# Optimization experiments

Measured on AMD Instinct MI355X. Metric: run time of the kernel, lower is better.

Reference implementation:

```python
import jax, jax.numpy as jnp
import numpy as np

IN_FEATURES = 8192
OUT_FEATURES = 14336
M_TOKENS = 64


def _dequant_rowwise_int4(w_packed, w_scales):
    # w_packed: [out, in//2], each byte holds two signed int4 values
    # (low nibble = even k index, high nibble = odd k index, two's complement)
    low = w_packed & 0xF
    high = (w_packed >> 4) & 0xF
    q = jnp.stack([low, high], axis=-1).reshape(w_packed.shape[0], -1)  # [out, in]
    q = jnp.where(q >= 8, q - 16, q).astype(jnp.float32)
    return q * w_scales[:, None]  # [out, in]


def setup_inputs() -> dict:
    key = jax.random.key(0)
    k1, k2, k3, k4 = jax.random.split(key, 4)
    x = jax.random.normal(k1, (M_TOKENS, IN_FEATURES), dtype=jnp.float32)
    w_packed = jax.random.randint(k2, (OUT_FEATURES, IN_FEATURES // 2), 0, 256, dtype=jnp.int32)
    # per-row scales, small positive values as produced by max-abs/7 quantization
    w_scales = jax.random.uniform(k3, (OUT_FEATURES,), dtype=jnp.float32) * 0.02 + 1e-4
    bias = jax.random.normal(k4, (OUT_FEATURES,), dtype=jnp.float32)
    return {"x": x, "w_packed": w_packed, "w_scales": w_scales, "bias": bias}


def reference(x, w_packed, w_scales, bias):
    original_shape = x.shape[:-1]
    x_2d = x.reshape(-1, IN_FEATURES)
    w = _dequant_rowwise_int4(w_packed, w_scales)  # [out, in]
    y = x_2d @ w.T + bias[None, :]  # [M, out]
    return y.reshape(*original_shape, OUT_FEATURES)
```

## Files before the change

### kernel.cpp

```cpp
#include <hip/hip_runtime.h>

#define IN_F   8192
#define OUT_F  14336
#define M_TOK  64
#define KPI    4096
#define BN     128
#define NBLK   (OUT_F / BN)
#define KSPLIT 8
#define KCHUNK (IN_F / KSPLIT)
#define BK     64
#define NSTEP  (KCHUNK / BK)
#define PSTRIDE (M_TOK * OUT_F)

typedef __attribute__((ext_vector_type(8)))  short bf16x8;
typedef __attribute__((ext_vector_type(16))) float f32x16;

__device__ __forceinline__ unsigned short f2bf_rne(float f) {
    unsigned u = __builtin_bit_cast(unsigned, f);
    u += 0x7FFFu + ((u >> 16) & 1u);
    return (unsigned short)(u >> 16);
}

__global__ __launch_bounds__(256) void qlin_prep(const float* __restrict__ x,
                                                 unsigned short* __restrict__ xb) {
    int gid = blockIdx.x * 256 + threadIdx.x;
    float4 v = reinterpret_cast<const float4*>(x)[gid];
    ushort4 o;
    o.x = f2bf_rne(v.x);
    o.y = f2bf_rne(v.y);
    o.z = f2bf_rne(v.z);
    o.w = f2bf_rne(v.w);
    reinterpret_cast<ushort4*>(xb)[gid] = o;
}

__device__ __forceinline__ int unpack2_bf16(int v) {
    int q0 = ((int)((unsigned)v << 28)) >> 28;
    int q1 = ((int)((unsigned)v << 24)) >> 28;
    unsigned u0 = __builtin_bit_cast(unsigned, (float)q0);
    unsigned u1 = __builtin_bit_cast(unsigned, (float)q1);
    return (int)((u0 >> 16) | (u1 & 0xFFFF0000u));
}

__device__ __forceinline__ bf16x8 unpack_b(int4 wv) {
    int4 pk;
    pk.x = unpack2_bf16(wv.x);
    pk.y = unpack2_bf16(wv.y);
    pk.z = unpack2_bf16(wv.z);
    pk.w = unpack2_bf16(wv.w);
    return __builtin_bit_cast(bf16x8, pk);
}

__device__ __forceinline__ void gload_lds16(const void* g, void* l) {
    __builtin_amdgcn_global_load_lds(
        (const __attribute__((address_space(1))) unsigned int*)g,
        (__attribute__((address_space(3))) unsigned int*)l,
        16, 0, 0);
}

__global__ __launch_bounds__(256) void qlin_gemm(const unsigned short* __restrict__ xb,
                                                 const int* __restrict__ wp,
                                                 const float* __restrict__ scales,
                                                 float* __restrict__ part) {
    __shared__ int            wlds[2][BN * (BK / 2)];
    __shared__ unsigned short xlds[2][M_TOK * BK];

    const int tid  = threadIdx.x;
    const int wave = tid >> 6;
    const int lane = tid & 63;
    const int tp   = lane & 31;
    const int qp   = lane >> 5;

    const int nblk = blockIdx.x % NBLK;
    const int kblk = blockIdx.x / NBLK;
    const int n0   = nblk * BN;
    const int kb   = kblk * KCHUNK;

    f32x16 acc0 = {0.f,0.f,0.f,0.f,0.f,0.f,0.f,0.f,0.f,0.f,0.f,0.f,0.f,0.f,0.f,0.f};
    f32x16 acc1 = acc0;

#define STAGE(b, t) do {                                                           \
    _Pragma("unroll")                                                              \
    for (int j = 0; j < 4; ++j) {                                                  \
        int li = (wave * 4 + j) * 64 + lane;                     \
        int r  = li >> 3;                                   \
        int cg = (li & 7) ^ (r & 7);                  \
        const int* gp = wp + (size_t)(n0 + r) * KPI + (kb >> 1) + (t) * (BK / 2) + cg * 4; \
        gload_lds16(gp, (char*)&wlds[b][0] + (size_t)li * 16);                     \
    }                                                                              \
    _Pragma("unroll")                                                              \
    for (int j = 0; j < 2; ++j) {                                                  \
        int li = (wave * 2 + j) * 64 + lane;                      \
        int r  = li >> 3;                                         \
        int cg = (li & 7) ^ (r & 7);                                               \
        const unsigned short* gp = xb + (size_t)r * IN_F + kb + (t) * BK + cg * 8; \
        gload_lds16(gp, (char*)&xlds[b][0] + (size_t)li * 16);                     \
    }                                                                              \
} while (0)

#define COMPUTE(b) do {                                                            \
    _Pragma("unroll")                                                              \
    for (int kf = 0; kf < 4; ++kf) {                                               \
        const int c = kf * 2 + qp;                      \
        const int R = wave * 32 + tp;                                              \
        int4 wv = *reinterpret_cast<const int4*>(                                  \
            (const char*)&wlds[b][0] + (size_t)(R * 8 + (c ^ (R & 7))) * 16);      \
        bf16x8 bb = unpack_b(wv);                                                  \
        bf16x8 a0 = *reinterpret_cast<const bf16x8*>(                              \
            (const char*)&xlds[b][0] + (size_t)(tp * 8 + (c ^ (tp & 7))) * 16);    \
        bf16x8 a1 = *reinterpret_cast<const bf16x8*>(                              \
            (const char*)&xlds[b][0] + (size_t)((32 + tp) * 8 + (c ^ (tp & 7))) * 16); \
        acc0 = __builtin_amdgcn_mfma_f32_32x32x16_bf16(a0, bb, acc0, 0, 0, 0);     \
        acc1 = __builtin_amdgcn_mfma_f32_32x32x16_bf16(a1, bb, acc1, 0, 0, 0);     \
    }                                                                              \
} while (0)

    STAGE(0, 0);
    STAGE(1, 1);

    for (int t = 0; t < NSTEP - 1; ++t) {
        const int cur = t & 1;
        asm volatile("s_waitcnt vmcnt(6)" ::: "memory");
        __builtin_amdgcn_sched_barrier(0);
        __builtin_amdgcn_s_barrier();
        __builtin_amdgcn_sched_barrier(0);
        COMPUTE(cur);
        __builtin_amdgcn_sched_barrier(0);
        __builtin_amdgcn_s_barrier();
        __builtin_amdgcn_sched_barrier(0);
        if (t + 2 < NSTEP) STAGE(cur, t + 2);
    }
    asm volatile("s_waitcnt vmcnt(0)" ::: "memory");
    __builtin_amdgcn_sched_barrier(0);
    __builtin_amdgcn_s_barrier();
    __builtin_amdgcn_sched_barrier(0);
    COMPUTE((NSTEP - 1) & 1);

    const int   n  = n0 + wave * 32 + tp;
    const float sc = scales[n];
    float* p = part + (size_t)kblk * PSTRIDE;
#pragma unroll
    for (int reg = 0; reg < 16; ++reg) {
        int m = (reg & 3) + 8 * (reg >> 2) + 4 * qp;
        p[(size_t)m        * OUT_F + n] = acc0[reg] * sc;
        p[(size_t)(32 + m) * OUT_F + n] = acc1[reg] * sc;
    }
#undef STAGE
#undef COMPUTE
}

__global__ __launch_bounds__(256) void qlin_reduce(const float* __restrict__ part,
                                                   const float* __restrict__ bias,
                                                   float* __restrict__ out) {
    const int    nq   = blockIdx.x * 256 + threadIdx.x;
    const int    m    = blockIdx.y;
    const size_t base = (size_t)m * (OUT_F / 4) + nq;
    float4 acc = reinterpret_cast<const float4*>(bias)[nq];
#pragma unroll
    for (int s = 0; s < KSPLIT; ++s) {
        float4 v = reinterpret_cast<const float4*>(part)[(size_t)s * (PSTRIDE / 4) + base];
        acc.x += v.x; acc.y += v.y; acc.z += v.z; acc.w += v.w;
    }
    reinterpret_cast<float4*>(out)[base] = acc;
}

extern "C" void kernel_launch(void* const* d_in, const int* in_sizes, int n_in,
                              void* d_out, int out_size, void* d_ws, size_t ws_size,
                              hipStream_t stream) {
    const float* x    = (const float*)d_in[0];
    const int*   wp   = (const int*)d_in[1];
    const float* sc   = (const float*)d_in[2];
    const float* bias = (const float*)d_in[3];
    float* out = (float*)d_out;

    unsigned short* xb   = (unsigned short*)d_ws;
    float*          part = (float*)((char*)d_ws + (1 << 20));

    qlin_prep<<<(M_TOK * IN_F) / 4 / 256, 256, 0, stream>>>(x, xb);
    qlin_gemm<<<NBLK * KSPLIT, 256, 0, stream>>>(xb, wp, sc, part);
    qlin_reduce<<<dim3(OUT_F / 4 / 256, M_TOK), 256, 0, stream>>>(part, bias, out);
}
```

Baseline: 354.1 us.

## Replace split-K partial buffer and reduce kernel with atomic accumulation into output

The GEMM blocks now atomically add their scaled partial results straight into the output, which a merged setup kernel pre-initialises with the bias alongside the bf16 conversion of x. This removes the separate reduce kernel and the write and read of a large partial-sum buffer. K-split is doubled to 16 to put more blocks in flight. The cost is more atomic traffic to the output, and the summation order is no longer deterministic.

```diff
diff --git a/kernel.cpp b/kernel.cpp
--- a/kernel.cpp
+++ b/kernel.cpp
@@ -6,11 +6,12 @@
 #define KPI    4096
 #define BN     128
 #define NBLK   (OUT_F / BN)
-#define KSPLIT 8
+#define KSPLIT 16
 #define KCHUNK (IN_F / KSPLIT)
 #define BK     64
 #define NSTEP  (KCHUNK / BK)
-#define PSTRIDE (M_TOK * OUT_F)
+#define XB_BLOCKS ((M_TOK * IN_F) / 4 / 256)
+#define OI_BLOCKS ((M_TOK * OUT_F) / 4 / 256)
 
 typedef __attribute__((ext_vector_type(8)))  short bf16x8;
 typedef __attribute__((ext_vector_type(16))) float f32x16;
@@ -21,16 +22,27 @@
     return (unsigned short)(u >> 16);
 }
 
-__global__ __launch_bounds__(256) void qlin_prep(const float* __restrict__ x,
-                                                 unsigned short* __restrict__ xb) {
-    int gid = blockIdx.x * 256 + threadIdx.x;
-    float4 v = reinterpret_cast<const float4*>(x)[gid];
-    ushort4 o;
-    o.x = f2bf_rne(v.x);
-    o.y = f2bf_rne(v.y);
-    o.z = f2bf_rne(v.z);
-    o.w = f2bf_rne(v.w);
-    reinterpret_cast<ushort4*>(xb)[gid] = o;
+__global__ __launch_bounds__(256) void qlin_setup(const float* __restrict__ x,
+                                                  const float* __restrict__ bias,
+                                                  unsigned short* __restrict__ xb,
+                                                  float* __restrict__ out) {
+    const int b   = blockIdx.x;
+    const int tid = threadIdx.x;
+    if (b < XB_BLOCKS) {
+        int gid = b * 256 + tid;
+        float4 v = reinterpret_cast<const float4*>(x)[gid];
+        ushort4 o;
+        o.x = f2bf_rne(v.x);
+        o.y = f2bf_rne(v.y);
+        o.z = f2bf_rne(v.z);
+        o.w = f2bf_rne(v.w);
+        reinterpret_cast<ushort4*>(xb)[gid] = o;
+    } else {
+        int idx = (b - XB_BLOCKS) * 256 + tid;
+        int nq  = idx % (OUT_F / 4);
+        reinterpret_cast<float4*>(out)[idx] =
+            reinterpret_cast<const float4*>(bias)[nq];
+    }
 }
 
 __device__ __forceinline__ int unpack2_bf16(int v) {
@@ -60,7 +72,7 @@
 __global__ __launch_bounds__(256) void qlin_gemm(const unsigned short* __restrict__ xb,
                                                  const int* __restrict__ wp,
                                                  const float* __restrict__ scales,
-                                                 float* __restrict__ part) {
+                                                 float* __restrict__ out) {
     __shared__ int            wlds[2][BN * (BK / 2)];
     __shared__ unsigned short xlds[2][M_TOK * BK];
 
@@ -137,30 +149,14 @@
 
     const int   n  = n0 + wave * 32 + tp;
     const float sc = scales[n];
-    float* p = part + (size_t)kblk * PSTRIDE;
 #pragma unroll
     for (int reg = 0; reg < 16; ++reg) {
         int m = (reg & 3) + 8 * (reg >> 2) + 4 * qp;
-        p[(size_t)m        * OUT_F + n] = acc0[reg] * sc;
-        p[(size_t)(32 + m) * OUT_F + n] = acc1[reg] * sc;
+        unsafeAtomicAdd(out + (size_t)m        * OUT_F + n, acc0[reg] * sc);
+        unsafeAtomicAdd(out + (size_t)(32 + m) * OUT_F + n, acc1[reg] * sc);
     }
 #undef STAGE
 #undef COMPUTE
-}
-
-__global__ __launch_bounds__(256) void qlin_reduce(const float* __restrict__ part,
-                                                   const float* __restrict__ bias,
-                                                   float* __restrict__ out) {
-    const int    nq   = blockIdx.x * 256 + threadIdx.x;
-    const int    m    = blockIdx.y;
-    const size_t base = (size_t)m * (OUT_F / 4) + nq;
-    float4 acc = reinterpret_cast<const float4*>(bias)[nq];
-#pragma unroll
-    for (int s = 0; s < KSPLIT; ++s) {
-        float4 v = reinterpret_cast<const float4*>(part)[(size_t)s * (PSTRIDE / 4) + base];
-        acc.x += v.x; acc.y += v.y; acc.z += v.z; acc.w += v.w;
-    }
-    reinterpret_cast<float4*>(out)[base] = acc;
 }
 
 extern "C" void kernel_launch(void* const* d_in, const int* in_sizes, int n_in,
@@ -172,10 +168,8 @@
     const float* bias = (const float*)d_in[3];
     float* out = (float*)d_out;
 
-    unsigned short* xb   = (unsigned short*)d_ws;
-    float*          part = (float*)((char*)d_ws + (1 << 20));
+    unsigned short* xb = (unsigned short*)d_ws;
 
-    qlin_prep<<<(M_TOK * IN_F) / 4 / 256, 256, 0, stream>>>(x, xb);
-    qlin_gemm<<<NBLK * KSPLIT, 256, 0, stream>>>(xb, wp, sc, part);
-    qlin_reduce<<<dim3(OUT_F / 4 / 256, M_TOK), 256, 0, stream>>>(part, bias, out);
+    qlin_setup<<<XB_BLOCKS + OI_BLOCKS, 256, 0, stream>>>(x, bias, xb, out);
+    qlin_gemm<<<NBLK * KSPLIT, 256, 0, stream>>>(xb, wp, sc, out);
 }
```

New measurement: 346.2 us. 2.2% less time.
